# Performance work log

Measured on AMD Instinct MI355X. Metric: run time of the kernel, lower is better.

Reference implementation:

```python
import jax, jax.numpy as jnp
import numpy as np

F_NUM = 22528
L1, L2, L3 = 3072, 15, 32
COUNT = 8
PSQT = 8
MAXF = 32
B = 4096


def _select(stacked, ls_idx, out_features):
    # stacked: [B, COUNT*out_features] -> pick the bucket row per sample
    r = stacked.reshape(stacked.shape[0], COUNT, out_features)
    return jnp.take_along_axis(r, ls_idx[:, None, None], axis=1)[:, 0, :]


def setup_inputs() -> dict:
    key = jax.random.key(0)
    ks = jax.random.split(key, 16)
    D = L1 + PSQT
    inp = {
        'us': jax.random.uniform(ks[0], (B, 1), jnp.float32),
        'them': None,
        'white_indices': jax.random.randint(ks[1], (B, MAXF), 0, F_NUM),
        'white_values': jax.random.uniform(ks[2], (B, MAXF), jnp.float32),
        'black_indices': jax.random.randint(ks[3], (B, MAXF), 0, F_NUM),
        'black_values': jax.random.uniform(ks[4], (B, MAXF), jnp.float32),
        'psqt_indices': jax.random.randint(ks[5], (B,), 0, PSQT),
        'layer_stack_indices': jax.random.randint(ks[6], (B,), 0, COUNT),
    }
    inp['them'] = 1.0 - inp['us']
    # parameters
    inp['ft_weight'] = jax.random.normal(ks[7], (F_NUM, D), jnp.float32) * 0.01
    inp['ft_bias'] = jax.random.normal(ks[8], (D,), jnp.float32) * 0.01
    inp['l1_w'] = jax.random.normal(ks[9], (COUNT * (L2 + 1), L1), jnp.float32) * 0.02
    inp['l1_b'] = jax.random.normal(ks[10], (COUNT * (L2 + 1),), jnp.float32) * 0.02
    inp['l1f_w'] = jax.random.normal(ks[11], (L2 + 1, L1), jnp.float32) * 0.02
    inp['l1f_b'] = jax.random.normal(ks[12], (L2 + 1,), jnp.float32) * 0.02
    inp['l2_w'] = jax.random.normal(ks[13], (COUNT * L3, 2 * L2), jnp.float32) * 0.1
    inp['l2_b'] = jax.random.normal(ks[14], (COUNT * L3,), jnp.float32) * 0.1
    inp['out_w'] = jax.random.normal(ks[15], (COUNT * 1, L3), jnp.float32) * 0.1
    inp['out_b'] = jnp.zeros((COUNT * 1,), jnp.float32)
    return inp


def reference(us, them, white_indices, white_values, black_indices, black_values,
              psqt_indices, layer_stack_indices, ft_weight, ft_bias,
              l1_w, l1_b, l1f_w, l1f_b, l2_w, l2_b, out_w, out_b):
    # DoubleFeatureTransformerSlice: sparse embedding accumulation
    wp = jnp.einsum('bmd,bm->bd', ft_weight[white_indices], white_values) + ft_bias
    bp = jnp.einsum('bmd,bm->bd', ft_weight[black_indices], black_values) + ft_bias
    w, wpsqt = wp[:, :L1], wp[:, L1:]
    b, bpsqt = bp[:, :L1], bp[:, L1:]
    l0 = us * jnp.concatenate([w, b], 1) + them * jnp.concatenate([b, w], 1)
    l0 = jnp.clip(l0, 0.0, 1.0)
    h = L1 // 2
    s0, s1, s2, s3 = l0[:, :h], l0[:, h:2*h], l0[:, 2*h:3*h], l0[:, 3*h:]
    l0 = jnp.concatenate([s0 * s1, s2 * s3], 1) * (127.0 / 128.0)  # [B, L1]
    wps = jnp.take_along_axis(wpsqt, psqt_indices[:, None], axis=1)
    bps = jnp.take_along_axis(bpsqt, psqt_indices[:, None], axis=1)
    # LayerStacks (dense over all buckets, then gather)
    mw = l1_w + jnp.tile(l1f_w, (COUNT, 1))
    mb = l1_b + jnp.tile(l1f_b, (COUNT,))
    l1c = _select(l0 @ mw.T + mb, layer_stack_indices, L2 + 1)
    l1x, l1x_out = l1c[:, :L2], l1c[:, L2:]
    l1x = jnp.clip(jnp.concatenate([jnp.square(l1x) * (127.0 / 128.0), l1x], 1), 0.0, 1.0)
    l2c = _select(l1x @ l2_w.T + l2_b, layer_stack_indices, L3)
    l2x = jnp.clip(l2c, 0.0, 1.0)
    l3c = _select(l2x @ out_w.T + out_b, layer_stack_indices, 1)
    x = l3c + l1x_out
    return x + (wps - bps) * (us - 0.5)
```

## Files before the change

kernel.cpp:

```cpp
#include <hip/hip_runtime.h>
#include <hip/hip_fp16.h>


#define DTOT 3080
#define TBL16_BYTES 138772480ull
#define MW_BYTES    1572864ull

constexpr float kScale = 127.0f / 128.0f;

__device__ __forceinline__ float clip01(float x) { return fminf(fmaxf(x, 0.0f), 1.0f); }

__device__ __forceinline__ void fma4(float4& a, float s, const float4 v) {
    a.x += s * v.x; a.y += s * v.y; a.z += s * v.z; a.w += s * v.w;
}

__device__ __forceinline__ float4 mix_clip(float u, float th, const float4 w, const float4 b) {
    float4 r;
    r.x = clip01(u * w.x + th * b.x);
    r.y = clip01(u * w.y + th * b.y);
    r.z = clip01(u * w.z + th * b.z);
    r.w = clip01(u * w.w + th * b.w);
    return r;
}

__device__ __forceinline__ float4 mul_scale(const float4 a, const float4 b) {
    float4 r;
    r.x = a.x * b.x * kScale;
    r.y = a.y * b.y * kScale;
    r.z = a.z * b.z * kScale;
    r.w = a.w * b.w * kScale;
    return r;
}

__device__ __forceinline__ void acc_unit(float4& Aa, float4& Ab, const uint4 raw, float v) {
    const __half2* h = (const __half2*)&raw;
    const float2 q0 = __half22float2(h[0]);
    const float2 q1 = __half22float2(h[1]);
    const float2 q2 = __half22float2(h[2]);
    const float2 q3 = __half22float2(h[3]);
    Aa.x += v * q0.x; Aa.y += v * q0.y; Aa.z += v * q1.x; Aa.w += v * q1.y;
    Ab.x += v * q2.x; Ab.y += v * q2.y; Ab.z += v * q3.x; Ab.w += v * q3.y;
}

__global__ __launch_bounds__(256) void convert_tbl(const unsigned long long* __restrict__ in,
                                                   uint2* __restrict__ out, int n4)
{
    union Un { unsigned long long u[2]; float f[4]; };
    union Pk { __half2 h2[2]; uint2 u2; };
    for (int i = blockIdx.x * 256 + threadIdx.x; i < n4; i += gridDim.x * 256) {
        Un v;
        v.u[0] = __builtin_nontemporal_load(&in[2 * (size_t)i]);
        v.u[1] = __builtin_nontemporal_load(&in[2 * (size_t)i + 1]);
        Pk p;
        p.h2[0] = __floats2half2_rn(v.f[0], v.f[1]);
        p.h2[1] = __floats2half2_rn(v.f[2], v.f[3]);
        out[i] = p.u2;
    }
}

__global__ __launch_bounds__(256) void merge_l1(const float* __restrict__ l1w,
                                                const float* __restrict__ l1fw,
                                                float* __restrict__ mw)
{
    const int idx = blockIdx.x * 256 + threadIdx.x;
    const float4* a = (const float4*)l1w;
    const float4* f = (const float4*)l1fw;
    float4* o = (float4*)mw;
    const int row = idx / 768;
    const int k = row & 15;
    const int col = idx - row * 768;
    const float4 x = a[idx];
    const float4 y = f[k * 768 + col];
    float4 r;
    r.x = x.x + y.x; r.y = x.y + y.y; r.z = x.z + y.z; r.w = x.w + y.w;
    o[idx] = r;
}

__global__ __launch_bounds__(128) void nnue_gather(
    const int* __restrict__ wi, const float* __restrict__ wv,
    const int* __restrict__ bi, const float* __restrict__ bv,
    const __half* __restrict__ tbl, const float* __restrict__ ftb,
    float4* __restrict__ acc_ws)
{
    const int blk = blockIdx.x;
    const int b = blk >> 3;
    const int s = blk & 7;
    const int t = threadIdx.x;

    __shared__ int   sidx[64];
    __shared__ float sval[64];
    if (t < 32)      { sidx[t] = wi[b * 32 + t];      sval[t] = wv[b * 32 + t]; }
    else if (t < 64) { sidx[t] = bi[b * 32 + t - 32]; sval[t] = bv[b * 32 + t - 32]; }
    __syncthreads();

    const int lo = 96 * s + (s < 2 ? s : 2);
    const int size = (s < 2) ? 97 : 96;
    if (t >= size) return;

    const int u = lo + t;
    const bool cb = (u >= 385);
    const int p = cb ? (u - 385) : u;

    const float4* fb4 = (const float4*)ftb;
    float4 Aa = fb4[2 * p], Ab = fb4[2 * p + 1];

    #pragma unroll 4
    for (int m = 0; m < 32; ++m) {
        const int row = cb ? sidx[32 + m] : sidx[m];
        const float v = cb ? sval[32 + m] : sval[m];
        const uint4 raw = ((const uint4*)(tbl + (size_t)row * DTOT))[p];
        acc_unit(Aa, Ab, raw, v);
    }

    float4* dst = acc_ws + ((size_t)b * 1540 + 2 * u);
    dst[0] = Aa; dst[1] = Ab;
}

__global__ __launch_bounds__(256) void nnue_mlp(
    const float* __restrict__ us_arr, const float* __restrict__ them_arr,
    const int* __restrict__ pidx, const int* __restrict__ lsidx,
    const float4* __restrict__ acc_ws, const float* __restrict__ mw,
    const float* __restrict__ l1b, const float* __restrict__ l1fb,
    const float* __restrict__ l2w, const float* __restrict__ l2b,
    const float* __restrict__ ow, const float* __restrict__ ob,
    float* __restrict__ out)
{
    const int b = blockIdx.x;
    const int t = threadIdx.x;

    __shared__ float red[4][16];
    __shared__ float l1c[16];
    __shared__ float l1x[30];

    const float usv = us_arr[b];
    const float thv = them_arr[b];
    const int ls = lsidx[b];
    const float4* acc = acc_ws + (size_t)b * 1540;
    const float4* mwbase = (const float4*)mw + (size_t)ls * 16 * 768;

    const int lane = t & 63;
    const int wave = t >> 6;

    float4 fvv[3];
    #pragma unroll
    for (int i = 0; i < 3; ++i) {
        const int col = t + 256 * i;
        const int q = (col >= 384) ? (col - 384) : col;
        const float4 W0 = acc[q],       W1 = acc[q + 384];
        const float4 B0 = acc[770 + q], B1 = acc[770 + q + 384];
        fvv[i] = (col >= 384)
            ? mul_scale(mix_clip(usv, thv, B0, W0), mix_clip(usv, thv, B1, W1))
            : mul_scale(mix_clip(usv, thv, W0, B0), mix_clip(usv, thv, W1, B1));
    }

    #pragma unroll
    for (int half = 0; half < 2; ++half) {
        float acck[8];
        #pragma unroll
        for (int k = 0; k < 8; ++k) acck[k] = 0.f;

        #pragma unroll
        for (int i = 0; i < 3; ++i) {
            const int col = t + 256 * i;
            const float4 fv = fvv[i];
            #pragma unroll
            for (int k = 0; k < 8; ++k) {
                const float4 w1 = mwbase[(size_t)(half * 8 + k) * 768 + col];
                acck[k] += fv.x * w1.x + fv.y * w1.y + fv.z * w1.z + fv.w * w1.w;
            }
        }

        #pragma unroll
        for (int k = 0; k < 8; ++k) {
            #pragma unroll
            for (int off = 32; off > 0; off >>= 1)
                acck[k] += __shfl_xor(acck[k], off, 64);
        }
        if (lane == 0) {
            #pragma unroll
            for (int k = 0; k < 8; ++k) red[wave][half * 8 + k] = acck[k];
        }
    }
    __syncthreads();

    if (t < 16) {
        l1c[t] = red[0][t] + red[1][t] + red[2][t] + red[3][t]
               + l1b[ls * 16 + t] + l1fb[t];
    }
    __syncthreads();

    if (t < 15) {
        const float v = l1c[t];
        l1x[t]      = clip01(v * v * kScale);
        l1x[15 + t] = clip01(v);
    }
    __syncthreads();

    float partial = 0.f;
    if (t < 32) {
        const float* r2 = l2w + (size_t)(ls * 32 + t) * 30;
        float s2 = l2b[ls * 32 + t];
        #pragma unroll
        for (int i = 0; i < 30; ++i) s2 += l1x[i] * r2[i];
        partial = clip01(s2) * ow[ls * 32 + t];
    }
    #pragma unroll
    for (int off = 16; off > 0; off >>= 1)
        partial += __shfl_xor(partial, off, 64);

    if (t == 0) {
        const int pi = pidx[b];
        const float* pw = (const float*)(acc + 768);
        const float* pb = (const float*)(acc + 1538);
        out[b] = partial + ob[ls] + l1c[15]
               + (pw[pi] - pb[pi]) * (usv - 0.5f);
    }
}

__global__ __launch_bounds__(512, 2) void nnue_fp16(
    const float* __restrict__ us_arr, const float* __restrict__ them_arr,
    const int* __restrict__ wi, const float* __restrict__ wv,
    const int* __restrict__ bi, const float* __restrict__ bv,
    const int* __restrict__ pidx, const int* __restrict__ lsidx,
    const __half* __restrict__ tbl, const float* __restrict__ ftb,
    const float* __restrict__ mw,
    const float* __restrict__ l1b, const float* __restrict__ l1fb,
    const float* __restrict__ l2w, const float* __restrict__ l2b,
    const float* __restrict__ ow, const float* __restrict__ ob,
    float* __restrict__ out)
{
    const int b = blockIdx.x;
    const int t = threadIdx.x;

    __shared__ float4 lds_acc[1540];
    __shared__ int   sidx[64];
    __shared__ float sval[64];
    __shared__ float red[4][16];
    __shared__ float l1c[16];
    __shared__ float l1x[30];

    if (t < 32)      { sidx[t] = wi[b * 32 + t];      sval[t] = wv[b * 32 + t]; }
    else if (t < 64) { sidx[t] = bi[b * 32 + t - 32]; sval[t] = bv[b * 32 + t - 32]; }
    __syncthreads();

    const int u0 = t;
    const bool c0 = (u0 >= 385);
    const int p0 = c0 ? (u0 - 385) : u0;
    const bool has1 = (t < 258);
    const int p1 = t + 127;

    const float4* fb4 = (const float4*)ftb;
    float4 A0a = fb4[2 * p0], A0b = fb4[2 * p0 + 1];
    float4 A1a = has1 ? fb4[2 * p1] : float4{0.f, 0.f, 0.f, 0.f};
    float4 A1b = has1 ? fb4[2 * p1 + 1] : float4{0.f, 0.f, 0.f, 0.f};

    #pragma unroll 4
    for (int m = 0; m < 32; ++m) {
        const __half* rowW = tbl + (size_t)sidx[m]      * DTOT;
        const __half* rowB = tbl + (size_t)sidx[32 + m] * DTOT;
        const float vw = sval[m], vb = sval[32 + m];

        const float v0 = c0 ? vb : vw;
        const uint4 raw0 = ((const uint4*)(c0 ? rowB : rowW))[p0];
        acc_unit(A0a, A0b, raw0, v0);
        if (has1) {
            const uint4 raw1 = ((const uint4*)rowB)[p1];
            acc_unit(A1a, A1b, raw1, vb);
        }
    }

    {
        const int g0 = (c0 ? 770 : 0) + 2 * p0;
        lds_acc[g0] = A0a; lds_acc[g0 + 1] = A0b;
        if (has1) {
            const int g1 = 770 + 2 * p1;
            lds_acc[g1] = A1a; lds_acc[g1 + 1] = A1b;
        }
    }
    __syncthreads();

    const float usv = us_arr[b];
    const float thv = them_arr[b];
    const int ls = lsidx[b];
    const float4* mwbase = (const float4*)mw + (size_t)ls * 16 * 768;

    const int lane = t & 63;
    const int wave = t >> 6;

    if (t < 256) {
        float4 fvv[3];
        #pragma unroll
        for (int i = 0; i < 3; ++i) {
            const int col = t + 256 * i;
            const int q = (col >= 384) ? (col - 384) : col;
            const float4 W0 = lds_acc[q],       W1 = lds_acc[q + 384];
            const float4 B0 = lds_acc[770 + q], B1 = lds_acc[770 + q + 384];
            fvv[i] = (col >= 384)
                ? mul_scale(mix_clip(usv, thv, B0, W0), mix_clip(usv, thv, B1, W1))
                : mul_scale(mix_clip(usv, thv, W0, B0), mix_clip(usv, thv, W1, B1));
        }

        #pragma unroll
        for (int half = 0; half < 2; ++half) {
            float acck[8];
            #pragma unroll
            for (int k = 0; k < 8; ++k) acck[k] = 0.f;

            #pragma unroll
            for (int i = 0; i < 3; ++i) {
                const int col = t + 256 * i;
                const float4 fv = fvv[i];
                #pragma unroll
                for (int k = 0; k < 8; ++k) {
                    const float4 w1 = mwbase[(size_t)(half * 8 + k) * 768 + col];
                    acck[k] += fv.x * w1.x + fv.y * w1.y + fv.z * w1.z + fv.w * w1.w;
                }
            }

            #pragma unroll
            for (int k = 0; k < 8; ++k) {
                #pragma unroll
                for (int off = 32; off > 0; off >>= 1)
                    acck[k] += __shfl_xor(acck[k], off, 64);
            }
            if (lane == 0) {
                #pragma unroll
                for (int k = 0; k < 8; ++k) red[wave][half * 8 + k] = acck[k];
            }
        }
    }
    __syncthreads();

    if (t < 16) {
        l1c[t] = red[0][t] + red[1][t] + red[2][t] + red[3][t]
               + l1b[ls * 16 + t] + l1fb[t];
    }
    __syncthreads();

    if (t < 15) {
        const float v = l1c[t];
        l1x[t]      = clip01(v * v * kScale);
        l1x[15 + t] = clip01(v);
    }
    __syncthreads();

    float partial = 0.f;
    if (t < 32) {
        const float* r2 = l2w + (size_t)(ls * 32 + t) * 30;
        float s2 = l2b[ls * 32 + t];
        #pragma unroll
        for (int i = 0; i < 30; ++i) s2 += l1x[i] * r2[i];
        partial = clip01(s2) * ow[ls * 32 + t];
    }
    #pragma unroll
    for (int off = 16; off > 0; off >>= 1)
        partial += __shfl_xor(partial, off, 64);

    if (t == 0) {
        const int pi = pidx[b];
        const float* pw = (const float*)&lds_acc[768];
        const float* pb = (const float*)&lds_acc[770 + 768];
        out[b] = partial + ob[ls] + l1c[15]
               + (pw[pi] - pb[pi]) * (usv - 0.5f);
    }
}

__global__ __launch_bounds__(512, 2) void nnue_fused(
    const float* __restrict__ us_arr, const float* __restrict__ them_arr,
    const int* __restrict__ wi, const float* __restrict__ wv,
    const int* __restrict__ bi, const float* __restrict__ bv,
    const int* __restrict__ pidx, const int* __restrict__ lsidx,
    const float* __restrict__ ftw, const float* __restrict__ ftb,
    const float* __restrict__ l1w, const float* __restrict__ l1b,
    const float* __restrict__ l1fw, const float* __restrict__ l1fb,
    const float* __restrict__ l2w, const float* __restrict__ l2b,
    const float* __restrict__ ow, const float* __restrict__ ob,
    float* __restrict__ out)
{
    const int b = blockIdx.x;
    const int t = threadIdx.x;

    __shared__ float4 lds_acc[1540];
    __shared__ int   sidx[64];
    __shared__ float sval[64];
    __shared__ float red[4][16];
    __shared__ float l1c[16];
    __shared__ float l1x[30];

    if (t < 32)      { sidx[t] = wi[b * 32 + t];      sval[t] = wv[b * 32 + t]; }
    else if (t < 64) { sidx[t] = bi[b * 32 + t - 32]; sval[t] = bv[b * 32 + t - 32]; }
    __syncthreads();

    const int g0 = t, g1 = t + 512, g2 = t + 1024;
    const int c1 = (g1 >= 770);
    const int s0 = t;
    const int s1 = c1 ? (g1 - 770) : g1;
    const int s2 = g2 - 770;
    const bool has3 = (t < 4);
    const int s3 = 766 + t;

    const float4* fb4 = (const float4*)ftb;
    float4 a0 = fb4[s0], a1 = fb4[s1], a2 = fb4[s2];
    float4 a3 = has3 ? fb4[s3] : float4{0.f, 0.f, 0.f, 0.f};

    #pragma unroll 2
    for (int m = 0; m < 32; ++m) {
        const float4* rw = (const float4*)(ftw + (size_t)sidx[m]      * DTOT);
        const float4* rb = (const float4*)(ftw + (size_t)sidx[32 + m] * DTOT);
        const float vw = sval[m], vb = sval[32 + m];

        fma4(a0, vw, rw[s0]);
        const float4* p1 = c1 ? rb : rw;
        fma4(a1, c1 ? vb : vw, p1[s1]);
        fma4(a2, vb, rb[s2]);
        if (has3) fma4(a3, vb, rb[s3]);
    }

    lds_acc[g0] = a0;
    lds_acc[g1] = a1;
    lds_acc[g2] = a2;
    if (has3) lds_acc[1536 + t] = a3;
    __syncthreads();

    const float usv = us_arr[b];
    const float thv = them_arr[b];
    const int ls = lsidx[b];

    const float4* w1base = (const float4*)(l1w + (size_t)ls * 16 * 3072);
    const float4* w2base = (const float4*)l1fw;

    const int lane = t & 63;
    const int wave = t >> 6;

    if (t < 256) {
        float acc[16];
        #pragma unroll
        for (int k = 0; k < 16; ++k) acc[k] = 0.f;

        #pragma unroll
        for (int i = 0; i < 3; ++i) {
            const int col = t + 256 * i;
            const int q = (col >= 384) ? (col - 384) : col;
            const float4 W0 = lds_acc[q],       W1 = lds_acc[q + 384];
            const float4 B0 = lds_acc[770 + q], B1 = lds_acc[770 + q + 384];
            const float4 fv = (col >= 384)
                ? mul_scale(mix_clip(usv, thv, B0, W0), mix_clip(usv, thv, B1, W1))
                : mul_scale(mix_clip(usv, thv, W0, B0), mix_clip(usv, thv, W1, B1));
            #pragma unroll
            for (int k = 0; k < 16; ++k) {
                const float4 w1 = w1base[(size_t)k * 768 + col];
                const float4 w2 = w2base[(size_t)k * 768 + col];
                acc[k] += fv.x * (w1.x + w2.x) + fv.y * (w1.y + w2.y)
                        + fv.z * (w1.z + w2.z) + fv.w * (w1.w + w2.w);
            }
        }

        #pragma unroll
        for (int k = 0; k < 16; ++k) {
            #pragma unroll
            for (int off = 32; off > 0; off >>= 1)
                acc[k] += __shfl_xor(acc[k], off, 64);
        }
        if (lane == 0) {
            #pragma unroll
            for (int k = 0; k < 16; ++k) red[wave][k] = acc[k];
        }
    }
    __syncthreads();

    if (t < 16) {
        l1c[t] = red[0][t] + red[1][t] + red[2][t] + red[3][t]
               + l1b[ls * 16 + t] + l1fb[t];
    }
    __syncthreads();

    if (t < 15) {
        const float v = l1c[t];
        l1x[t]      = clip01(v * v * kScale);
        l1x[15 + t] = clip01(v);
    }
    __syncthreads();

    float partial = 0.f;
    if (t < 32) {
        const float* r2 = l2w + (size_t)(ls * 32 + t) * 30;
        float s2 = l2b[ls * 32 + t];
        #pragma unroll
        for (int i = 0; i < 30; ++i) s2 += l1x[i] * r2[i];
        partial = clip01(s2) * ow[ls * 32 + t];
    }
    #pragma unroll
    for (int off = 16; off > 0; off >>= 1)
        partial += __shfl_xor(partial, off, 64);

    if (t == 0) {
        const int pi = pidx[b];
        const float* pw = (const float*)&lds_acc[768];
        const float* pb = (const float*)&lds_acc[770 + 768];
        out[b] = partial + ob[ls] + l1c[15]
               + (pw[pi] - pb[pi]) * (usv - 0.5f);
    }
}

extern "C" void kernel_launch(void* const* d_in, const int* in_sizes, int n_in,
                              void* d_out, int out_size, void* d_ws, size_t ws_size,
                              hipStream_t stream) {
    const float* us   = (const float*)d_in[0];
    const float* them = (const float*)d_in[1];
    const int*   wi   = (const int*)d_in[2];
    const float* wv   = (const float*)d_in[3];
    const int*   bi   = (const int*)d_in[4];
    const float* bv   = (const float*)d_in[5];
    const int*   pidx = (const int*)d_in[6];
    const int*   ls   = (const int*)d_in[7];
    const float* ftw  = (const float*)d_in[8];
    const float* ftb  = (const float*)d_in[9];
    const float* l1w  = (const float*)d_in[10];
    const float* l1b  = (const float*)d_in[11];
    const float* l1fw = (const float*)d_in[12];
    const float* l1fb = (const float*)d_in[13];
    const float* l2w  = (const float*)d_in[14];
    const float* l2b  = (const float*)d_in[15];
    const float* ow   = (const float*)d_in[16];
    const float* ob   = (const float*)d_in[17];
    float* out = (float*)d_out;

    const int B = in_sizes[0];
    const size_t acc_bytes = (size_t)B * 1540 * 16;
    const size_t need_fp16 = TBL16_BYTES + MW_BYTES;
    const size_t need_full = need_fp16 + acc_bytes;

    if (ws_size >= need_full) {
        __half* tbl16 = (__half*)d_ws;
        float*  mw    = (float*)((char*)d_ws + TBL16_BYTES);
        float4* accw  = (float4*)((char*)d_ws + TBL16_BYTES + MW_BYTES);
        convert_tbl<<<2048, 256, 0, stream>>>((const unsigned long long*)ftw, (uint2*)d_ws, 17346560);
        merge_l1<<<384, 256, 0, stream>>>(l1w, l1fw, mw);
        nnue_gather<<<B * 8, 128, 0, stream>>>(wi, wv, bi, bv, tbl16, ftb, accw);
        nnue_mlp<<<B, 256, 0, stream>>>(us, them, pidx, ls, accw, mw,
                                        l1b, l1fb, l2w, l2b, ow, ob, out);
    } else if (ws_size >= need_fp16) {
        __half* tbl16 = (__half*)d_ws;
        float*  mw    = (float*)((char*)d_ws + TBL16_BYTES);
        convert_tbl<<<2048, 256, 0, stream>>>((const unsigned long long*)ftw, (uint2*)d_ws, 17346560);
        merge_l1<<<384, 256, 0, stream>>>(l1w, l1fw, mw);
        nnue_fp16<<<B, 512, 0, stream>>>(us, them, wi, wv, bi, bv, pidx, ls,
                                         tbl16, ftb, mw, l1b, l1fb,
                                         l2w, l2b, ow, ob, out);
    } else {
        nnue_fused<<<B, 512, 0, stream>>>(us, them, wi, wv, bi, bv, pidx, ls,
                                          ftw, ftb, l1w, l1b, l1fw, l1fb,
                                          l2w, l2b, ow, ob, out);
    }
}
```

Measured before the change: 349.3 us.

## Partition gather by column slice per XCC with atomic work-stealing scheduler

The gather kernel now assigns each of 8 column slices of the fp16 feature table to a preferred XCC, read from the hardware register, with blocks claiming items through per-slice atomic counters and stealing from other slices when their own is exhausted. The aim is to keep each XCC's L2 working set to one eighth of the table columns. Each block handles 4 samples and computes white and black accumulations together in one thread, which doubles memory-level parallelism per thread. This adds a memset, atomic contention, and a dependency on the XCC-ID register semantics.

```diff
diff --git a/kernel.cpp b/kernel.cpp
--- a/kernel.cpp
+++ b/kernel.cpp
@@ -76,44 +76,70 @@
     o[idx] = r;
 }
 
-__global__ __launch_bounds__(128) void nnue_gather(
+__global__ __launch_bounds__(256) void nnue_gather(
     const int* __restrict__ wi, const float* __restrict__ wv,
     const int* __restrict__ bi, const float* __restrict__ bv,
     const __half* __restrict__ tbl, const float* __restrict__ ftb,
-    float4* __restrict__ acc_ws)
+    float4* __restrict__ acc_ws, int* __restrict__ cnt, int NI)
 {
-    const int blk = blockIdx.x;
-    const int b = blk >> 3;
-    const int s = blk & 7;
+    __shared__ int   s_item;
+    __shared__ int   sidx[4][64];
+    __shared__ float sval[4][64];
+
+    if (threadIdx.x == 0) {
+        unsigned int xid;
+        asm volatile("s_getreg_b32 %0, hwreg(HW_REG_XCC_ID)" : "=s"(xid));
+        xid &= 7;
+        int item = -1;
+        for (int k = 0; k < 8; ++k) {
+            const int s = (xid + k) & 7;
+            const int c = atomicAdd(&cnt[s], 1);
+            if (c < NI) { item = s * NI + c; break; }
+        }
+        s_item = item;
+    }
+    __syncthreads();
+    const int item = s_item;
+    if (item < 0) return;
+
+    const int s = item / NI;
+    const int bbase = (item - s * NI) * 4;
+    const int w_lo = (s == 0) ? 0 : (48 * s + 1);
+    const int nw   = (s == 0) ? 49 : 48;
+
     const int t = threadIdx.x;
-
-    __shared__ int   sidx[64];
-    __shared__ float sval[64];
-    if (t < 32)      { sidx[t] = wi[b * 32 + t];      sval[t] = wv[b * 32 + t]; }
-    else if (t < 64) { sidx[t] = bi[b * 32 + t - 32]; sval[t] = bv[b * 32 + t - 32]; }
-    __syncthreads();
-
-    const int lo = 96 * s + (s < 2 ? s : 2);
-    const int size = (s < 2) ? 97 : 96;
-    if (t >= size) return;
-
-    const int u = lo + t;
-    const bool cb = (u >= 385);
-    const int p = cb ? (u - 385) : u;
-
-    const float4* fb4 = (const float4*)ftb;
-    float4 Aa = fb4[2 * p], Ab = fb4[2 * p + 1];
-
-    #pragma unroll 4
-    for (int m = 0; m < 32; ++m) {
-        const int row = cb ? sidx[32 + m] : sidx[m];
-        const float v = cb ? sval[32 + m] : sval[m];
-        const uint4 raw = ((const uint4*)(tbl + (size_t)row * DTOT))[p];
-        acc_unit(Aa, Ab, raw, v);
-    }
-
-    float4* dst = acc_ws + ((size_t)b * 1540 + 2 * u);
-    dst[0] = Aa; dst[1] = Ab;
+    const int bl = t >> 6;
+    const int t64 = t & 63;
+    {
+        const int b = bbase + bl;
+        sidx[bl][t64] = (t64 < 32) ? wi[b * 32 + t64] : bi[b * 32 + (t64 - 32)];
+        sval[bl][t64] = (t64 < 32) ? wv[b * 32 + t64] : bv[b * 32 + (t64 - 32)];
+    }
+    __syncthreads();
+
+    if (t64 < nw) {
+        const int b = bbase + bl;
+        const int w = w_lo + t64;
+        const float4* fb4 = (const float4*)ftb;
+        const float4 bias_a = fb4[2 * w], bias_b = fb4[2 * w + 1];
+        float4 Wa = bias_a, Wb = bias_b;
+        float4 Ba = bias_a, Bb = bias_b;
+
+        #pragma unroll 4
+        for (int m = 0; m < 32; ++m) {
+            const int   rw = sidx[bl][m];      const float vw = sval[bl][m];
+            const int   rb = sidx[bl][32 + m]; const float vb = sval[bl][32 + m];
+            const uint4 rawW = ((const uint4*)(tbl + (size_t)rw * DTOT))[w];
+            const uint4 rawB = ((const uint4*)(tbl + (size_t)rb * DTOT))[w];
+            acc_unit(Wa, Wb, rawW, vw);
+            acc_unit(Ba, Bb, rawB, vb);
+        }
+
+        float4* dst = acc_ws + (size_t)b * 1540;
+        dst[2 * w]     = Wa;  dst[2 * w + 1]     = Wb;
+        const int ub = 385 + w;
+        dst[2 * ub]    = Ba;  dst[2 * ub + 1]    = Bb;
+    }
 }
 
 __global__ __launch_bounds__(256) void nnue_mlp(
@@ -528,15 +554,19 @@
     const int B = in_sizes[0];
     const size_t acc_bytes = (size_t)B * 1540 * 16;
     const size_t need_fp16 = TBL16_BYTES + MW_BYTES;
-    const size_t need_full = need_fp16 + acc_bytes;
-
-    if (ws_size >= need_full) {
+    const size_t cnt_off   = need_fp16 + acc_bytes;
+    const size_t need_full = cnt_off + 64;
+
+    if (ws_size >= need_full && (B & 3) == 0) {
         __half* tbl16 = (__half*)d_ws;
         float*  mw    = (float*)((char*)d_ws + TBL16_BYTES);
-        float4* accw  = (float4*)((char*)d_ws + TBL16_BYTES + MW_BYTES);
+        float4* accw  = (float4*)((char*)d_ws + need_fp16);
+        int*    cnt   = (int*)((char*)d_ws + cnt_off);
+        const int NI = B / 4;
+        hipMemsetAsync(cnt, 0, 32, stream);
         convert_tbl<<<2048, 256, 0, stream>>>((const unsigned long long*)ftw, (uint2*)d_ws, 17346560);
         merge_l1<<<384, 256, 0, stream>>>(l1w, l1fw, mw);
-        nnue_gather<<<B * 8, 128, 0, stream>>>(wi, wv, bi, bv, tbl16, ftb, accw);
+        nnue_gather<<<8 * NI, 256, 0, stream>>>(wi, wv, bi, bv, tbl16, ftb, accw, cnt, NI);
         nnue_mlp<<<B, 256, 0, stream>>>(us, them, pidx, ls, accw, mw,
                                         l1b, l1fb, l2w, l2b, ow, ob, out);
     } else if (ws_size >= need_fp16) {
```

New measurement: 348.9 us. No clear change (-0.1%).
